# Kernel tuning notes

Hardware: AMD Instinct MI355X
Metric: run time of the kernel (lower is better)

Reference implementation:

```python
import jax, jax.numpy as jnp
import numpy as np

N, D, T = 4096, 512, 4096
TEMPERATURE = 0.07
MARGIN = 0.5
CONT_WEIGHT = 1.0
TRIP_WEIGHT = 0.3
EPS = 1e-8        # eps in the log / denominator (matches torch code)
PD_EPS = 1e-6     # F.pairwise_distance default eps added to the difference


def setup_inputs() -> dict:
    key = jax.random.key(0)
    k1, k2, k3 = jax.random.split(key, 3)
    embeddings = jax.random.normal(k1, (N, D), dtype=jnp.float32)
    labels = jax.random.randint(k2, (N,), 0, 256)            # ~16 positives per place
    triplets = jax.random.randint(k3, (T, 3), 0, N)          # (anchor, pos, neg) indices
    return {"embeddings": embeddings, "labels": labels, "triplets": triplets}


def reference(embeddings, labels, triplets):
    # ---- MultiPositiveContrastiveLoss ----
    # F.cosine_similarity normalizes each row with eps=1e-8 on the norm.
    norms = jnp.linalg.norm(embeddings, axis=1, keepdims=True)
    n_emb = embeddings / jnp.maximum(norms, EPS)
    sim = (n_emb @ n_emb.T) / TEMPERATURE                    # [N, N]

    pos_mask = (labels[:, None] == labels[None, :]).astype(embeddings.dtype)
    pos_mask = pos_mask * (1.0 - jnp.eye(sim.shape[0], dtype=embeddings.dtype))

    exp_sim = jnp.exp(sim)
    pos_sum = (exp_sim * pos_mask).sum(axis=1)
    total_sum = exp_sim.sum(axis=1)
    loss = -jnp.log(pos_sum / (total_sum + EPS) + EPS)

    valid = pos_mask.sum(axis=1) > 0
    cnt = valid.sum()
    cont_loss = jnp.where(
        cnt > 0,
        jnp.where(valid, loss, 0.0).sum() / jnp.maximum(cnt, 1).astype(loss.dtype),
        jnp.zeros((), loss.dtype),
    )

    # ---- TripletLoss, vectorized over all triplets (replaces Python loop) ----
    a = embeddings[triplets[:, 0]]   # [T, D]
    p = embeddings[triplets[:, 1]]
    ng = embeddings[triplets[:, 2]]
    pos_dist = jnp.linalg.norm(a - p + PD_EPS, axis=1)
    neg_dist = jnp.linalg.norm(a - ng + PD_EPS, axis=1)
    trip_loss = jnp.maximum(pos_dist - neg_dist + MARGIN, 0.0).mean()

    total = CONT_WEIGHT * cont_loss + TRIP_WEIGHT * trip_loss
    return (total, cont_loss, trip_loss)
```

## Files before the change

### kernel.cpp

```cpp
#include <hip/hip_runtime.h>

#define NN 4096
#define DD 512
#define TT 4096

typedef __bf16 bf16x8 __attribute__((ext_vector_type(8)));
typedef float f32x4 __attribute__((ext_vector_type(4)));

constexpr float INV_TEMP = 1.0f / 0.07f;

#define AS1(p) ((__attribute__((address_space(1))) const void*)(p))
#define AS3(p) ((__attribute__((address_space(3))) void*)(p))

__global__ __launch_bounds__(256) void k_normtrip(const float* __restrict__ emb,
                                                  __bf16* __restrict__ nemb,
                                                  const int* __restrict__ trip,
                                                  float* __restrict__ tl) {
    int wave = threadIdx.x >> 6, lane = threadIdx.x & 63;
    int row = blockIdx.x * 4 + wave;

    int ia = trip[row * 3 + 0], ip = trip[row * 3 + 1], ig = trip[row * 3 + 2];
    const float4* pa = (const float4*)(emb + (size_t)ia * DD);
    const float4* pp = (const float4*)(emb + (size_t)ip * DD);
    const float4* pn = (const float4*)(emb + (size_t)ig * DD);
    float d1 = 0.0f, d2 = 0.0f;
    #pragma unroll
    for (int j = 0; j < 2; ++j) {
        float4 a = pa[lane * 2 + j];
        float4 p = pp[lane * 2 + j];
        float4 n = pn[lane * 2 + j];
        float dx;
        dx = a.x - p.x + 1e-6f; d1 += dx * dx;
        dx = a.y - p.y + 1e-6f; d1 += dx * dx;
        dx = a.z - p.z + 1e-6f; d1 += dx * dx;
        dx = a.w - p.w + 1e-6f; d1 += dx * dx;
        dx = a.x - n.x + 1e-6f; d2 += dx * dx;
        dx = a.y - n.y + 1e-6f; d2 += dx * dx;
        dx = a.z - n.z + 1e-6f; d2 += dx * dx;
        dx = a.w - n.w + 1e-6f; d2 += dx * dx;
    }

    const float4* src = (const float4*)(emb + (size_t)row * DD);
    float4 x0 = src[lane * 2 + 0];
    float4 x1 = src[lane * 2 + 1];
    float ss = x0.x * x0.x + x0.y * x0.y + x0.z * x0.z + x0.w * x0.w +
               x1.x * x1.x + x1.y * x1.y + x1.z * x1.z + x1.w * x1.w;
    #pragma unroll
    for (int m = 1; m < 64; m <<= 1) ss += __shfl_xor(ss, m, 64);
    float inv = 1.0f / fmaxf(sqrtf(ss), 1e-8f);
    bf16x8 v;
    v[0] = (__bf16)(x0.x * inv); v[1] = (__bf16)(x0.y * inv);
    v[2] = (__bf16)(x0.z * inv); v[3] = (__bf16)(x0.w * inv);
    v[4] = (__bf16)(x1.x * inv); v[5] = (__bf16)(x1.y * inv);
    v[6] = (__bf16)(x1.z * inv); v[7] = (__bf16)(x1.w * inv);
    *(bf16x8*)(nemb + (size_t)row * DD + lane * 8) = v;

    #pragma unroll
    for (int m = 1; m < 64; m <<= 1) {
        d1 += __shfl_xor(d1, m, 64);
        d2 += __shfl_xor(d2, m, 64);
    }
    if (lane == 0) tl[row] = fmaxf(sqrtf(d1) - sqrtf(d2) + 0.5f, 0.0f);
}


#define VMW(N) asm volatile("s_waitcnt vmcnt(" #N ")" ::: "memory")
#define NOVM ((void)0)

#define STAGE_A(T, H) do { \
    __builtin_amdgcn_global_load_lds(AS1(gA0 + (size_t)((H) * 128) * DD + (T) * 64), \
                                     AS3(lA0 + (((T) & 1) * 2 + (H)) * 8192), 16, 0, 0); \
    __builtin_amdgcn_global_load_lds(AS1(gA0 + (size_t)((H) * 128 + 8) * DD + (T) * 64), \
                                     AS3(lA0 + (((T) & 1) * 2 + (H)) * 8192 + 512), 16, 0, 0); \
} while (0)

#define STAGE_B(T, H) do { \
    __builtin_amdgcn_global_load_lds(AS1(gB0 + (size_t)((H) * 128) * DD + (T) * 64), \
                                     AS3(lB0 + (((T) & 1) * 2 + (H)) * 8192), 16, 0, 0); \
    __builtin_amdgcn_global_load_lds(AS1(gB0 + (size_t)((H) * 128 + 8) * DD + (T) * 64), \
                                     AS3(lB0 + (((T) & 1) * 2 + (H)) * 8192 + 512), 16, 0, 0); \
} while (0)

#define PHASE(PAR, LOADA, QM, QN, STAGE_STMT, VM_STMT) do { \
    const __bf16* aB_ = aSm + ((PAR) * 2 + (QM)) * 8192; \
    const __bf16* bB_ = bSm + ((PAR) * 2 + (QN)) * 8192; \
    if (LOADA) { \
        _Pragma("unroll") \
        for (int fm_ = 0; fm_ < 4; ++fm_) { \
            af[fm_][0] = *(const bf16x8*)(aB_ + fm_ * 1024 + rdA0); \
            af[fm_][1] = *(const bf16x8*)(aB_ + fm_ * 1024 + rdA1); \
        } \
    } \
    _Pragma("unroll") \
    for (int fn_ = 0; fn_ < 2; ++fn_) { \
        bfr[fn_][0] = *(const bf16x8*)(bB_ + fn_ * 1024 + rdB0); \
        bfr[fn_][1] = *(const bf16x8*)(bB_ + fn_ * 1024 + rdB1); \
    } \
    STAGE_STMT; \
    asm volatile("s_waitcnt lgkmcnt(0)" ::: "memory"); \
    __builtin_amdgcn_sched_barrier(0); \
    __builtin_amdgcn_s_setprio(1); \
    _Pragma("unroll") \
    for (int kc_ = 0; kc_ < 2; ++kc_) { \
        _Pragma("unroll") \
        for (int fm_ = 0; fm_ < 4; ++fm_) { \
            _Pragma("unroll") \
            for (int fn_ = 0; fn_ < 2; ++fn_) \
                acc[QM][QN][fm_][fn_] = __builtin_amdgcn_mfma_f32_16x16x32_bf16( \
                    af[fm_][kc_], bfr[fn_][kc_], acc[QM][QN][fm_][fn_], 0, 0, 0); \
        } \
    } \
    __builtin_amdgcn_s_setprio(0); \
    __builtin_amdgcn_sched_barrier(0); \
    VM_STMT; \
    asm volatile("" ::: "memory"); \
    __builtin_amdgcn_s_barrier(); \
} while (0)

#define GROUP(G, S12, S34, VM1, VM4) do { \
    PHASE((G) & 1, 1, 0, 0, { if (S12) STAGE_A((G) + 1, 1); }, VM1); \
    PHASE((G) & 1, 0, 0, 1, { if (S12) STAGE_B((G) + 1, 1); }, NOVM); \
    PHASE((G) & 1, 1, 1, 0, { if (S34) STAGE_A((G) + 2, 0); }, NOVM); \
    PHASE((G) & 1, 0, 1, 1, { if (S34) STAGE_B((G) + 2, 0); }, VM4); \
} while (0)

__global__ __launch_bounds__(512, 2) void k_contrast(const __bf16* __restrict__ nemb,
                                                     const int* __restrict__ labels,
                                                     float* __restrict__ posP,
                                                     float* __restrict__ totP,
                                                     float* __restrict__ cntP) {
    __shared__ __attribute__((aligned(16))) __bf16 aSm[4 * 8192];
    __shared__ __attribute__((aligned(16))) __bf16 bSm[4 * 8192];
    __shared__ int rlab[256];
    __shared__ int clab[256];

    int tid = threadIdx.x;
    int lane = tid & 63, wave = tid >> 6;
    int wr = wave >> 2, wc = wave & 3;
    int l15 = lane & 15, quad = lane >> 4;
    int swz = l15 & 7;

    int bid = blockIdx.x;
    int xcd = bid & 7, idx = bid >> 3;
    int rowblk = (xcd >> 1) * 4 + (idx >> 3);
    int colblk = (xcd & 1) * 8 + (idx & 7);
    int row0 = rowblk * 256, col0 = colblk * 256;

    if (tid < 256) rlab[tid] = labels[row0 + tid];
    else           clab[tid - 256] = labels[col0 + tid - 256];

    int srow = wave * 16 + ((tid >> 3) & 7);
    int scol = ((tid & 7) ^ ((tid >> 3) & 7)) * 8;
    const __bf16* gA0 = nemb + (size_t)(row0 + srow) * DD + scol;
    const __bf16* gB0 = nemb + (size_t)(col0 + srow) * DD + scol;
    __bf16* lA0 = aSm + wave * 1024 + (tid & 63) * 8;
    __bf16* lB0 = bSm + wave * 1024 + (tid & 63) * 8;

    int rdA0 = (wr * 64 + l15) * 64 + ((quad ^ swz) * 8);
    int rdA1 = (wr * 64 + l15) * 64 + (((4 + quad) ^ swz) * 8);
    int rdB0 = (wc * 32 + l15) * 64 + ((quad ^ swz) * 8);
    int rdB1 = (wc * 32 + l15) * 64 + (((4 + quad) ^ swz) * 8);

    f32x4 acc[2][2][4][2];
    #pragma unroll
    for (int a = 0; a < 2; ++a)
        #pragma unroll
        for (int b = 0; b < 2; ++b)
            #pragma unroll
            for (int c = 0; c < 4; ++c)
                #pragma unroll
                for (int d = 0; d < 2; ++d) {
                    f32x4 z = {0.0f, 0.0f, 0.0f, 0.0f};
                    acc[a][b][c][d] = z;
                }

    bf16x8 af[4][2], bfr[2][2];

    STAGE_A(0, 0); STAGE_B(0, 0);
    STAGE_A(0, 1); STAGE_B(0, 1);
    STAGE_A(1, 0); STAGE_B(1, 0);
    VMW(8);
    asm volatile("" ::: "memory");
    __builtin_amdgcn_s_barrier();

    GROUP(0, 1, 1, VMW(6), VMW(8));
    GROUP(1, 1, 1, VMW(6), VMW(8));
    GROUP(2, 1, 1, VMW(6), VMW(8));
    GROUP(3, 1, 1, VMW(6), VMW(8));
    GROUP(4, 1, 1, VMW(6), VMW(8));
    GROUP(5, 1, 1, VMW(6), VMW(8));
    GROUP(6, 1, 0, VMW(6), VMW(4));
    GROUP(7, 0, 0, VMW(0), NOVM);

    #pragma unroll
    for (int qm = 0; qm < 2; ++qm)
    #pragma unroll
    for (int fm = 0; fm < 4; ++fm) {
        int rloc = qm * 128 + wr * 64 + fm * 16 + quad * 4;
        int gibase = row0 + rloc;
        int rl[4];
        #pragma unroll
        for (int v = 0; v < 4; ++v) rl[v] = rlab[rloc + v];
        float tv[4] = {0, 0, 0, 0}, pv[4] = {0, 0, 0, 0}, cv[4] = {0, 0, 0, 0};
        #pragma unroll
        for (int qn = 0; qn < 2; ++qn)
        #pragma unroll
        for (int fn = 0; fn < 2; ++fn) {
            int cloc = qn * 128 + wc * 32 + fn * 16 + l15;
            int cl = clab[cloc];
            int gj = col0 + cloc;
            f32x4 a = acc[qm][qn][fm][fn];
            #pragma unroll
            for (int v = 0; v < 4; ++v) {
                float e = __expf(a[v] * INV_TEMP);
                tv[v] += e;
                bool match = (rl[v] == cl) && ((gibase + v) != gj);
                pv[v] += match ? e : 0.0f;
                cv[v] += match ? 1.0f : 0.0f;
            }
        }
        #pragma unroll
        for (int m = 1; m < 16; m <<= 1) {
            #pragma unroll
            for (int v = 0; v < 4; ++v) {
                tv[v] += __shfl_xor(tv[v], m, 64);
                pv[v] += __shfl_xor(pv[v], m, 64);
                cv[v] += __shfl_xor(cv[v], m, 64);
            }
        }
        if (l15 == 0) {
            #pragma unroll
            for (int v = 0; v < 4; ++v) {
                int o = (gibase + v) * 64 + colblk * 4 + wc;
                posP[o] = pv[v];
                totP[o] = tv[v];
                cntP[o] = cv[v];
            }
        }
    }
}

__global__ __launch_bounds__(256) void k_rowloss(const float* __restrict__ posP,
                                                 const float* __restrict__ totP,
                                                 const float* __restrict__ cntP,
                                                 float* __restrict__ rloss,
                                                 float* __restrict__ rvalid) {
    int wave = threadIdx.x >> 6, lane = threadIdx.x & 63;
    int row = blockIdx.x * 4 + wave;
    float p = posP[row * 64 + lane];
    float t = totP[row * 64 + lane];
    float c = cntP[row * 64 + lane];
    #pragma unroll
    for (int m = 1; m < 64; m <<= 1) {
        p += __shfl_xor(p, m, 64);
        t += __shfl_xor(t, m, 64);
        c += __shfl_xor(c, m, 64);
    }
    if (lane == 0) {
        float loss = -logf(p / (t + 1e-8f) + 1e-8f);
        bool valid = c > 0.0f;
        rloss[row] = valid ? loss : 0.0f;
        rvalid[row] = valid ? 1.0f : 0.0f;
    }
}

__global__ __launch_bounds__(256) void k_final(const float* __restrict__ rloss,
                                               const float* __restrict__ rvalid,
                                               const float* __restrict__ tl,
                                               float* __restrict__ out) {
    int tid = threadIdx.x;
    float sl = 0.0f, sv = 0.0f, st = 0.0f;
    for (int i = tid; i < NN; i += 256) {
        sl += rloss[i];
        sv += rvalid[i];
        st += tl[i];
    }
    #pragma unroll
    for (int m = 1; m < 64; m <<= 1) {
        sl += __shfl_xor(sl, m, 64);
        sv += __shfl_xor(sv, m, 64);
        st += __shfl_xor(st, m, 64);
    }
    __shared__ float red[3][4];
    int lane = tid & 63, wave = tid >> 6;
    if (lane == 0) { red[0][wave] = sl; red[1][wave] = sv; red[2][wave] = st; }
    __syncthreads();
    if (tid == 0) {
        float SL = red[0][0] + red[0][1] + red[0][2] + red[0][3];
        float SV = red[1][0] + red[1][1] + red[1][2] + red[1][3];
        float ST = red[2][0] + red[2][1] + red[2][2] + red[2][3];
        float cont = (SV > 0.0f) ? (SL / SV) : 0.0f;
        float trip = ST * (1.0f / (float)TT);
        out[0] = cont + 0.3f * trip;
        out[1] = cont;
        out[2] = trip;
    }
}

extern "C" void kernel_launch(void* const* d_in, const int* in_sizes, int n_in,
                              void* d_out, int out_size, void* d_ws, size_t ws_size,
                              hipStream_t stream) {
    const float* emb = (const float*)d_in[0];
    const int* labels = (const int*)d_in[1];
    const int* trips = (const int*)d_in[2];
    float* out = (float*)d_out;
    char* ws = (char*)d_ws;

    __bf16* nemb  = (__bf16*)(ws);
    float* posP   = (float*)(ws + 4194304);
    float* totP   = (float*)(ws + 5242880);
    float* cntP   = (float*)(ws + 6291456);
    float* rloss  = (float*)(ws + 7340032);
    float* rvalid = (float*)(ws + 7356416);
    float* tl     = (float*)(ws + 7372800);

    k_normtrip<<<NN / 4, 256, 0, stream>>>(emb, nemb, trips, tl);
    k_contrast<<<256, 512, 0, stream>>>(nemb, labels, posP, totP, cntP);
    k_rowloss<<<NN / 4, 256, 0, stream>>>(posP, totP, cntP, rloss, rvalid);
    k_final<<<1, 256, 0, stream>>>(rloss, rvalid, tl, out);
}
```

Baseline: 100.9 us.

## Restructure GEMM phases into fewer barriers and use atomic row reductions

The contrastive GEMM main loop is regrouped from four phases per k-step, each ending in a barrier, into three MFMA blocks with two barriers. Both B quarter-tiles are preloaded into registers, and the vmcnt waits are retuned to match. Per-row partial sums are now accumulated with float atomics straight into per-row buffers instead of being written to a 64-way partial array that a later kernel reduces. The positive count is recomputed from labels in the row-loss kernel, and the final reduction also uses atomics. This removes partial-buffer traffic and synchronization, at the cost of atomic contention, nondeterministic summation order and higher register pressure.

```diff
diff --git a/kernel.cpp b/kernel.cpp
--- a/kernel.cpp
+++ b/kernel.cpp
@@ -15,9 +15,15 @@
 __global__ __launch_bounds__(256) void k_normtrip(const float* __restrict__ emb,
                                                   __bf16* __restrict__ nemb,
                                                   const int* __restrict__ trip,
-                                                  float* __restrict__ tl) {
+                                                  float* __restrict__ tl,
+                                                  float* __restrict__ posR,
+                                                  float* __restrict__ totR,
+                                                  float* __restrict__ scal) {
     int wave = threadIdx.x >> 6, lane = threadIdx.x & 63;
     int row = blockIdx.x * 4 + wave;
+
+    if (lane == 0) { posR[row] = 0.0f; totR[row] = 0.0f; }
+    if (blockIdx.x == 0 && threadIdx.x < 3) scal[threadIdx.x] = 0.0f;
 
     int ia = trip[row * 3 + 0], ip = trip[row * 3 + 1], ig = trip[row * 3 + 2];
     const float4* pa = (const float4*)(emb + (size_t)ia * DD);
@@ -81,25 +87,7 @@
                                      AS3(lB0 + (((T) & 1) * 2 + (H)) * 8192 + 512), 16, 0, 0); \
 } while (0)
 
-#define PHASE(PAR, LOADA, QM, QN, STAGE_STMT, VM_STMT) do { \
-    const __bf16* aB_ = aSm + ((PAR) * 2 + (QM)) * 8192; \
-    const __bf16* bB_ = bSm + ((PAR) * 2 + (QN)) * 8192; \
-    if (LOADA) { \
-        _Pragma("unroll") \
-        for (int fm_ = 0; fm_ < 4; ++fm_) { \
-            af[fm_][0] = *(const bf16x8*)(aB_ + fm_ * 1024 + rdA0); \
-            af[fm_][1] = *(const bf16x8*)(aB_ + fm_ * 1024 + rdA1); \
-        } \
-    } \
-    _Pragma("unroll") \
-    for (int fn_ = 0; fn_ < 2; ++fn_) { \
-        bfr[fn_][0] = *(const bf16x8*)(bB_ + fn_ * 1024 + rdB0); \
-        bfr[fn_][1] = *(const bf16x8*)(bB_ + fn_ * 1024 + rdB1); \
-    } \
-    STAGE_STMT; \
-    asm volatile("s_waitcnt lgkmcnt(0)" ::: "memory"); \
-    __builtin_amdgcn_sched_barrier(0); \
-    __builtin_amdgcn_s_setprio(1); \
+#define MFMA_Q(QM, QN) do { \
     _Pragma("unroll") \
     for (int kc_ = 0; kc_ < 2; ++kc_) { \
         _Pragma("unroll") \
@@ -107,28 +95,63 @@
             _Pragma("unroll") \
             for (int fn_ = 0; fn_ < 2; ++fn_) \
                 acc[QM][QN][fm_][fn_] = __builtin_amdgcn_mfma_f32_16x16x32_bf16( \
-                    af[fm_][kc_], bfr[fn_][kc_], acc[QM][QN][fm_][fn_], 0, 0, 0); \
+                    af[fm_][kc_], bfr[QN][fn_][kc_], acc[QM][QN][fm_][fn_], 0, 0, 0); \
         } \
     } \
+} while (0)
+
+#define GROUP(G, S12, S34, VMTAIL) do { \
+    const __bf16* aB0 = aSm + (((G) & 1) * 2 + 0) * 8192; \
+    const __bf16* bB0 = bSm + (((G) & 1) * 2 + 0) * 8192; \
+    const __bf16* bB1 = bSm + (((G) & 1) * 2 + 1) * 8192; \
+    _Pragma("unroll") \
+    for (int fm_ = 0; fm_ < 4; ++fm_) { \
+        af[fm_][0] = *(const bf16x8*)(aB0 + fm_ * 1024 + rdA0); \
+        af[fm_][1] = *(const bf16x8*)(aB0 + fm_ * 1024 + rdA1); \
+    } \
+    _Pragma("unroll") \
+    for (int fn_ = 0; fn_ < 2; ++fn_) { \
+        bfr[0][fn_][0] = *(const bf16x8*)(bB0 + fn_ * 1024 + rdB0); \
+        bfr[0][fn_][1] = *(const bf16x8*)(bB0 + fn_ * 1024 + rdB1); \
+        bfr[1][fn_][0] = *(const bf16x8*)(bB1 + fn_ * 1024 + rdB0); \
+        bfr[1][fn_][1] = *(const bf16x8*)(bB1 + fn_ * 1024 + rdB1); \
+    } \
+    if (S12) STAGE_A((G) + 1, 1); \
+    asm volatile("s_waitcnt lgkmcnt(0)" ::: "memory"); \
+    __builtin_amdgcn_sched_barrier(0); \
+    __builtin_amdgcn_s_setprio(1); \
+    MFMA_Q(0, 0); \
     __builtin_amdgcn_s_setprio(0); \
+    asm volatile("" ::: "memory"); \
+    __builtin_amdgcn_s_barrier(); \
+    if (S12) STAGE_B((G) + 1, 1); \
+    __builtin_amdgcn_s_setprio(1); \
+    MFMA_Q(0, 1); \
+    __builtin_amdgcn_s_setprio(0); \
+    { \
+        const __bf16* aB1 = aSm + (((G) & 1) * 2 + 1) * 8192; \
+        _Pragma("unroll") \
+        for (int fm_ = 0; fm_ < 4; ++fm_) { \
+            af[fm_][0] = *(const bf16x8*)(aB1 + fm_ * 1024 + rdA0); \
+            af[fm_][1] = *(const bf16x8*)(aB1 + fm_ * 1024 + rdA1); \
+        } \
+    } \
+    if (S34) { STAGE_A((G) + 2, 0); STAGE_B((G) + 2, 0); } \
+    asm volatile("s_waitcnt lgkmcnt(0)" ::: "memory"); \
     __builtin_amdgcn_sched_barrier(0); \
-    VM_STMT; \
+    __builtin_amdgcn_s_setprio(1); \
+    MFMA_Q(1, 0); \
+    MFMA_Q(1, 1); \
+    __builtin_amdgcn_s_setprio(0); \
+    VMTAIL; \
     asm volatile("" ::: "memory"); \
     __builtin_amdgcn_s_barrier(); \
 } while (0)
 
-#define GROUP(G, S12, S34, VM1, VM4) do { \
-    PHASE((G) & 1, 1, 0, 0, { if (S12) STAGE_A((G) + 1, 1); }, VM1); \
-    PHASE((G) & 1, 0, 0, 1, { if (S12) STAGE_B((G) + 1, 1); }, NOVM); \
-    PHASE((G) & 1, 1, 1, 0, { if (S34) STAGE_A((G) + 2, 0); }, NOVM); \
-    PHASE((G) & 1, 0, 1, 1, { if (S34) STAGE_B((G) + 2, 0); }, VM4); \
-} while (0)
-
 __global__ __launch_bounds__(512, 2) void k_contrast(const __bf16* __restrict__ nemb,
                                                      const int* __restrict__ labels,
-                                                     float* __restrict__ posP,
-                                                     float* __restrict__ totP,
-                                                     float* __restrict__ cntP) {
+                                                     float* __restrict__ posR,
+                                                     float* __restrict__ totR) {
     __shared__ __attribute__((aligned(16))) __bf16 aSm[4 * 8192];
     __shared__ __attribute__((aligned(16))) __bf16 bSm[4 * 8192];
     __shared__ int rlab[256];
@@ -174,23 +197,23 @@
                     acc[a][b][c][d] = z;
                 }
 
-    bf16x8 af[4][2], bfr[2][2];
+    bf16x8 af[4][2], bfr[2][2][2];
 
     STAGE_A(0, 0); STAGE_B(0, 0);
     STAGE_A(0, 1); STAGE_B(0, 1);
     STAGE_A(1, 0); STAGE_B(1, 0);
-    VMW(8);
+    VMW(4);
     asm volatile("" ::: "memory");
     __builtin_amdgcn_s_barrier();
 
-    GROUP(0, 1, 1, VMW(6), VMW(8));
-    GROUP(1, 1, 1, VMW(6), VMW(8));
-    GROUP(2, 1, 1, VMW(6), VMW(8));
-    GROUP(3, 1, 1, VMW(6), VMW(8));
-    GROUP(4, 1, 1, VMW(6), VMW(8));
-    GROUP(5, 1, 1, VMW(6), VMW(8));
-    GROUP(6, 1, 0, VMW(6), VMW(4));
-    GROUP(7, 0, 0, VMW(0), NOVM);
+    GROUP(0, 1, 1, VMW(4));
+    GROUP(1, 1, 1, VMW(4));
+    GROUP(2, 1, 1, VMW(4));
+    GROUP(3, 1, 1, VMW(4));
+    GROUP(4, 1, 1, VMW(4));
+    GROUP(5, 1, 1, VMW(4));
+    GROUP(6, 1, 0, VMW(0));
+    GROUP(7, 0, 0, NOVM);
 
     #pragma unroll
     for (int qm = 0; qm < 2; ++qm)
@@ -201,7 +224,7 @@
         int rl[4];
         #pragma unroll
         for (int v = 0; v < 4; ++v) rl[v] = rlab[rloc + v];
-        float tv[4] = {0, 0, 0, 0}, pv[4] = {0, 0, 0, 0}, cv[4] = {0, 0, 0, 0};
+        float tv[4] = {0, 0, 0, 0}, pv[4] = {0, 0, 0, 0};
         #pragma unroll
         for (int qn = 0; qn < 2; ++qn)
         #pragma unroll
@@ -216,79 +239,53 @@
                 tv[v] += e;
                 bool match = (rl[v] == cl) && ((gibase + v) != gj);
                 pv[v] += match ? e : 0.0f;
-                cv[v] += match ? 1.0f : 0.0f;
             }
         }
         #pragma unroll
-        for (int m = 1; m < 16; m <<= 1) {
+        for (int m = 1; m < 4; m <<= 1) {
             #pragma unroll
             for (int v = 0; v < 4; ++v) {
                 tv[v] += __shfl_xor(tv[v], m, 64);
                 pv[v] += __shfl_xor(pv[v], m, 64);
-                cv[v] += __shfl_xor(cv[v], m, 64);
             }
         }
-        if (l15 == 0) {
+        if ((l15 & 3) == 0) {
             #pragma unroll
             for (int v = 0; v < 4; ++v) {
-                int o = (gibase + v) * 64 + colblk * 4 + wc;
-                posP[o] = pv[v];
-                totP[o] = tv[v];
-                cntP[o] = cv[v];
+                atomicAdd(&totR[gibase + v], tv[v]);
+                atomicAdd(&posR[gibase + v], pv[v]);
             }
         }
     }
 }
 
-__global__ __launch_bounds__(256) void k_rowloss(const float* __restrict__ posP,
-                                                 const float* __restrict__ totP,
-                                                 const float* __restrict__ cntP,
-                                                 float* __restrict__ rloss,
-                                                 float* __restrict__ rvalid) {
+__global__ __launch_bounds__(256) void k_rowloss(const float* __restrict__ posR,
+                                                 const float* __restrict__ totR,
+                                                 const int* __restrict__ labels,
+                                                 const float* __restrict__ tl,
+                                                 float* __restrict__ scal) {
     int wave = threadIdx.x >> 6, lane = threadIdx.x & 63;
     int row = blockIdx.x * 4 + wave;
-    float p = posP[row * 64 + lane];
-    float t = totP[row * 64 + lane];
-    float c = cntP[row * 64 + lane];
-    #pragma unroll
-    for (int m = 1; m < 64; m <<= 1) {
-        p += __shfl_xor(p, m, 64);
-        t += __shfl_xor(t, m, 64);
-        c += __shfl_xor(c, m, 64);
-    }
+    int myLab = labels[row];
+    int c = 0;
+    #pragma unroll 8
+    for (int j = lane; j < NN; j += 64) c += (labels[j] == myLab) ? 1 : 0;
+    #pragma unroll
+    for (int m = 1; m < 64; m <<= 1) c += __shfl_xor(c, m, 64);
     if (lane == 0) {
-        float loss = -logf(p / (t + 1e-8f) + 1e-8f);
-        bool valid = c > 0.0f;
-        rloss[row] = valid ? loss : 0.0f;
-        rvalid[row] = valid ? 1.0f : 0.0f;
-    }
-}
-
-__global__ __launch_bounds__(256) void k_final(const float* __restrict__ rloss,
-                                               const float* __restrict__ rvalid,
-                                               const float* __restrict__ tl,
-                                               float* __restrict__ out) {
-    int tid = threadIdx.x;
-    float sl = 0.0f, sv = 0.0f, st = 0.0f;
-    for (int i = tid; i < NN; i += 256) {
-        sl += rloss[i];
-        sv += rvalid[i];
-        st += tl[i];
-    }
-    #pragma unroll
-    for (int m = 1; m < 64; m <<= 1) {
-        sl += __shfl_xor(sl, m, 64);
-        sv += __shfl_xor(sv, m, 64);
-        st += __shfl_xor(st, m, 64);
-    }
-    __shared__ float red[3][4];
-    int lane = tid & 63, wave = tid >> 6;
-    if (lane == 0) { red[0][wave] = sl; red[1][wave] = sv; red[2][wave] = st; }
-    __syncthreads();
-    if (tid == 0) {
-        float SL = red[0][0] + red[0][1] + red[0][2] + red[0][3];
-        float SV = red[1][0] + red[1][1] + red[1][2] + red[1][3];
-        float ST = red[2][0] + red[2][1] + red[2][2] + red[2][3];
+        bool valid = c > 1;
+        float p = posR[row], t = totR[row];
+        float loss = valid ? -logf(p / (t + 1e-8f) + 1e-8f) : 0.0f;
+        atomicAdd(&scal[0], loss);
+        atomicAdd(&scal[1], valid ? 1.0f : 0.0f);
+        atomicAdd(&scal[2], tl[row]);
+    }
+}
+
+__global__ __launch_bounds__(64) void k_final(const float* __restrict__ scal,
+                                              float* __restrict__ out) {
+    if (threadIdx.x == 0) {
+        float SL = scal[0], SV = scal[1], ST = scal[2];
         float cont = (SV > 0.0f) ? (SL / SV) : 0.0f;
         float trip = ST * (1.0f / (float)TT);
         out[0] = cont + 0.3f * trip;
@@ -306,16 +303,14 @@
     float* out = (float*)d_out;
     char* ws = (char*)d_ws;
 
-    __bf16* nemb  = (__bf16*)(ws);
-    float* posP   = (float*)(ws + 4194304);
-    float* totP   = (float*)(ws + 5242880);
-    float* cntP   = (float*)(ws + 6291456);
-    float* rloss  = (float*)(ws + 7340032);
-    float* rvalid = (float*)(ws + 7356416);
-    float* tl     = (float*)(ws + 7372800);
-
-    k_normtrip<<<NN / 4, 256, 0, stream>>>(emb, nemb, trips, tl);
-    k_contrast<<<256, 512, 0, stream>>>(nemb, labels, posP, totP, cntP);
-    k_rowloss<<<NN / 4, 256, 0, stream>>>(posP, totP, cntP, rloss, rvalid);
-    k_final<<<1, 256, 0, stream>>>(rloss, rvalid, tl, out);
-}
+    __bf16* nemb = (__bf16*)(ws);
+    float* posR  = (float*)(ws + 4194304);
+    float* totR  = (float*)(ws + 4210688);
+    float* tl    = (float*)(ws + 4227072);
+    float* scal  = (float*)(ws + 4243456);
+
+    k_normtrip<<<NN / 4, 256, 0, stream>>>(emb, nemb, trips, tl, posR, totR, scal);
+    k_contrast<<<256, 512, 0, stream>>>(nemb, labels, posR, totR);
+    k_rowloss<<<NN / 4, 256, 0, stream>>>(posR, totR, labels, tl, scal);
+    k_final<<<1, 64, 0, stream>>>(scal, out);
+}
```

Result: slower. 358.2 us (+255.1%).

## Accumulate row sums with atomics and fuse row-loss into final reduction

Applied to the files above, without the earlier changes.

Instead of writing 64 per-row partials for pos/total/count and reducing them in a separate row-loss kernel, the contrastive kernel now reduces over 4 lanes and atomically adds into per-row pos/total accumulators that the norm kernel zeroes. The positive-count output is dropped; row validity is derived from a label histogram built in a single 1024-thread final kernel that also computes the per-row log loss. This removes one launch and the partial-buffer traffic, at the cost of many float atomics (nondeterministic summation order) and a serial single-block tail over 4096 rows.

```diff
diff --git a/kernel.cpp b/kernel.cpp
--- a/kernel.cpp
+++ b/kernel.cpp
@@ -15,9 +15,13 @@
 __global__ __launch_bounds__(256) void k_normtrip(const float* __restrict__ emb,
                                                   __bf16* __restrict__ nemb,
                                                   const int* __restrict__ trip,
-                                                  float* __restrict__ tl) {
+                                                  float* __restrict__ tl,
+                                                  float* __restrict__ posR,
+                                                  float* __restrict__ totR) {
     int wave = threadIdx.x >> 6, lane = threadIdx.x & 63;
     int row = blockIdx.x * 4 + wave;
+
+    if (lane == 0) { posR[row] = 0.0f; totR[row] = 0.0f; }
 
     int ia = trip[row * 3 + 0], ip = trip[row * 3 + 1], ig = trip[row * 3 + 2];
     const float4* pa = (const float4*)(emb + (size_t)ia * DD);
@@ -126,9 +130,8 @@
 
 __global__ __launch_bounds__(512, 2) void k_contrast(const __bf16* __restrict__ nemb,
                                                      const int* __restrict__ labels,
-                                                     float* __restrict__ posP,
-                                                     float* __restrict__ totP,
-                                                     float* __restrict__ cntP) {
+                                                     float* __restrict__ posR,
+                                                     float* __restrict__ totR) {
     __shared__ __attribute__((aligned(16))) __bf16 aSm[4 * 8192];
     __shared__ __attribute__((aligned(16))) __bf16 bSm[4 * 8192];
     __shared__ int rlab[256];
@@ -201,7 +204,7 @@
         int rl[4];
         #pragma unroll
         for (int v = 0; v < 4; ++v) rl[v] = rlab[rloc + v];
-        float tv[4] = {0, 0, 0, 0}, pv[4] = {0, 0, 0, 0}, cv[4] = {0, 0, 0, 0};
+        float tv[4] = {0, 0, 0, 0}, pv[4] = {0, 0, 0, 0};
         #pragma unroll
         for (int qn = 0; qn < 2; ++qn)
         #pragma unroll
@@ -216,64 +219,53 @@
                 tv[v] += e;
                 bool match = (rl[v] == cl) && ((gibase + v) != gj);
                 pv[v] += match ? e : 0.0f;
-                cv[v] += match ? 1.0f : 0.0f;
             }
         }
         #pragma unroll
-        for (int m = 1; m < 16; m <<= 1) {
+        for (int m = 1; m < 4; m <<= 1) {
             #pragma unroll
             for (int v = 0; v < 4; ++v) {
                 tv[v] += __shfl_xor(tv[v], m, 64);
                 pv[v] += __shfl_xor(pv[v], m, 64);
-                cv[v] += __shfl_xor(cv[v], m, 64);
             }
         }
-        if (l15 == 0) {
+        if ((l15 & 3) == 0) {
             #pragma unroll
             for (int v = 0; v < 4; ++v) {
-                int o = (gibase + v) * 64 + colblk * 4 + wc;
-                posP[o] = pv[v];
-                totP[o] = tv[v];
-                cntP[o] = cv[v];
+                atomicAdd(&totR[gibase + v], tv[v]);
+                atomicAdd(&posR[gibase + v], pv[v]);
             }
         }
     }
 }
 
-__global__ __launch_bounds__(256) void k_rowloss(const float* __restrict__ posP,
-                                                 const float* __restrict__ totP,
-                                                 const float* __restrict__ cntP,
-                                                 float* __restrict__ rloss,
-                                                 float* __restrict__ rvalid) {
-    int wave = threadIdx.x >> 6, lane = threadIdx.x & 63;
-    int row = blockIdx.x * 4 + wave;
-    float p = posP[row * 64 + lane];
-    float t = totP[row * 64 + lane];
-    float c = cntP[row * 64 + lane];
-    #pragma unroll
-    for (int m = 1; m < 64; m <<= 1) {
-        p += __shfl_xor(p, m, 64);
-        t += __shfl_xor(t, m, 64);
-        c += __shfl_xor(c, m, 64);
-    }
-    if (lane == 0) {
-        float loss = -logf(p / (t + 1e-8f) + 1e-8f);
-        bool valid = c > 0.0f;
-        rloss[row] = valid ? loss : 0.0f;
-        rvalid[row] = valid ? 1.0f : 0.0f;
-    }
-}
-
-__global__ __launch_bounds__(256) void k_final(const float* __restrict__ rloss,
-                                               const float* __restrict__ rvalid,
-                                               const float* __restrict__ tl,
-                                               float* __restrict__ out) {
+__global__ __launch_bounds__(1024) void k_rowfinal(const float* __restrict__ posR,
+                                                   const float* __restrict__ totR,
+                                                   const int* __restrict__ labels,
+                                                   const float* __restrict__ tl,
+                                                   float* __restrict__ out) {
+    __shared__ int hist[256];
+    __shared__ float red[3][16];
     int tid = threadIdx.x;
+    if (tid < 256) hist[tid] = 0;
+    __syncthreads();
+    int lab[4];
+    #pragma unroll
+    for (int j = 0; j < 4; ++j) {
+        lab[j] = labels[tid + j * 1024];
+        atomicAdd(&hist[lab[j]], 1);
+    }
+    __syncthreads();
     float sl = 0.0f, sv = 0.0f, st = 0.0f;
-    for (int i = tid; i < NN; i += 256) {
-        sl += rloss[i];
-        sv += rvalid[i];
-        st += tl[i];
+    #pragma unroll
+    for (int j = 0; j < 4; ++j) {
+        int row = tid + j * 1024;
+        bool valid = hist[lab[j]] > 1;
+        float p = posR[row], t = totR[row];
+        float loss = valid ? -logf(p / (t + 1e-8f) + 1e-8f) : 0.0f;
+        sl += loss;
+        sv += valid ? 1.0f : 0.0f;
+        st += tl[row];
     }
     #pragma unroll
     for (int m = 1; m < 64; m <<= 1) {
@@ -281,14 +273,13 @@
         sv += __shfl_xor(sv, m, 64);
         st += __shfl_xor(st, m, 64);
     }
-    __shared__ float red[3][4];
     int lane = tid & 63, wave = tid >> 6;
     if (lane == 0) { red[0][wave] = sl; red[1][wave] = sv; red[2][wave] = st; }
     __syncthreads();
     if (tid == 0) {
-        float SL = red[0][0] + red[0][1] + red[0][2] + red[0][3];
-        float SV = red[1][0] + red[1][1] + red[1][2] + red[1][3];
-        float ST = red[2][0] + red[2][1] + red[2][2] + red[2][3];
+        float SL = 0.0f, SV = 0.0f, ST = 0.0f;
+        #pragma unroll
+        for (int w = 0; w < 16; ++w) { SL += red[0][w]; SV += red[1][w]; ST += red[2][w]; }
         float cont = (SV > 0.0f) ? (SL / SV) : 0.0f;
         float trip = ST * (1.0f / (float)TT);
         out[0] = cont + 0.3f * trip;
@@ -306,16 +297,12 @@
     float* out = (float*)d_out;
     char* ws = (char*)d_ws;
 
-    __bf16* nemb  = (__bf16*)(ws);
-    float* posP   = (float*)(ws + 4194304);
-    float* totP   = (float*)(ws + 5242880);
-    float* cntP   = (float*)(ws + 6291456);
-    float* rloss  = (float*)(ws + 7340032);
-    float* rvalid = (float*)(ws + 7356416);
-    float* tl     = (float*)(ws + 7372800);
-
-    k_normtrip<<<NN / 4, 256, 0, stream>>>(emb, nemb, trips, tl);
-    k_contrast<<<256, 512, 0, stream>>>(nemb, labels, posP, totP, cntP);
-    k_rowloss<<<NN / 4, 256, 0, stream>>>(posP, totP, cntP, rloss, rvalid);
-    k_final<<<1, 256, 0, stream>>>(rloss, rvalid, tl, out);
+    __bf16* nemb = (__bf16*)(ws);
+    float* posR  = (float*)(ws + 4194304);
+    float* totR  = (float*)(ws + 4210688);
+    float* tl    = (float*)(ws + 4227072);
+
+    k_normtrip<<<NN / 4, 256, 0, stream>>>(emb, nemb, trips, tl, posR, totR);
+    k_contrast<<<256, 512, 0, stream>>>(nemb, labels, posR, totR);
+    k_rowfinal<<<1, 1024, 0, stream>>>(posR, totR, labels, tl, out);
 }
```

Result: slower. 183.3 us (+81.7%).
